# Kernel optimization log

Measured on AMD Instinct MI355X. Metric: run time of the kernel, lower is better.

Reference implementation:

```python
import jax, jax.numpy as jnp
import numpy as np

N, E, D_NODE, D_EDGE, H, NUM_CLASSES = 2048, 4096, 128, 128, 4, 16
SPARSE_RATIO = 0.5  # forward arg sparse_ratio; <1.0 triggers top-k node masking
NEG = jnp.float32(-1e9)


def _mha(x, wq, bq, wk, bk, wv, bv, wo, bo, mask):
    """Multi-head self-attention over tokens x [T, D]; mask broadcastable to [H, T, T]."""
    T, D = x.shape
    dh = D // H
    q = (x @ wq + bq).reshape(T, H, dh)
    k = (x @ wk + bk).reshape(T, H, dh)
    v = (x @ wv + bv).reshape(T, H, dh)
    scores = jnp.einsum('qhd,khd->hqk', q, k) * (1.0 / float(np.sqrt(dh)))
    scores = jnp.where(mask, scores, NEG)
    attn = jax.nn.softmax(scores, axis=-1)
    out = jnp.einsum('hqk,khd->qhd', attn, v).reshape(T, D)
    return out @ wo + bo


def setup_inputs() -> dict:
    key = jax.random.key(0)
    ks = jax.random.split(key, 20)
    f32 = jnp.float32
    def w(i, shape):
        return jax.random.normal(ks[i], shape, dtype=f32) * 0.02
    z = lambda *s: jnp.zeros(s, f32)
    return {
        'node_features': jax.random.normal(ks[0], (N, D_NODE), dtype=f32),
        'edge_features': jax.random.normal(ks[1], (E, D_EDGE), dtype=f32),
        'edge_index': jax.random.randint(ks[2], (2, E), 0, N),
        'w_rn': w(3, (D_NODE, 1)), 'b_rn': z(1),
        'w_re': w(4, (D_EDGE, 1)), 'b_re': z(1),
        'wq_n': w(5, (D_NODE, D_NODE)), 'bq_n': z(D_NODE),
        'wk_n': w(6, (D_NODE, D_NODE)), 'bk_n': z(D_NODE),
        'wv_n': w(7, (D_NODE, D_NODE)), 'bv_n': z(D_NODE),
        'wo_n': w(8, (D_NODE, D_NODE)), 'bo_n': z(D_NODE),
        'wq_e': w(9, (D_EDGE, D_EDGE)), 'bq_e': z(D_EDGE),
        'wk_e': w(10, (D_EDGE, D_EDGE)), 'bk_e': z(D_EDGE),
        'wv_e': w(11, (D_EDGE, D_EDGE)), 'bv_e': z(D_EDGE),
        'wo_e': w(12, (D_EDGE, D_EDGE)), 'bo_e': z(D_EDGE),
        'w_ne': w(13, (D_NODE, D_EDGE)), 'b_ne': z(D_EDGE),
        'w_c1': w(14, (D_EDGE, 2 * D_EDGE)), 'b_c1': z(2 * D_EDGE),
        'w_c2': w(15, (2 * D_EDGE, NUM_CLASSES)), 'b_c2': z(NUM_CLASSES),
    }


def reference(node_features, edge_features, edge_index,
              w_rn, b_rn, w_re, b_re,
              wq_n, bq_n, wk_n, bk_n, wv_n, bv_n, wo_n, bo_n,
              wq_e, bq_e, wk_e, bk_e, wv_e, bv_e, wo_e, bo_e,
              w_ne, b_ne, w_c1, b_c1, w_c2, b_c2):
    # Importance router: scalar sigmoid scores per node / edge
    node_scores = jax.nn.sigmoid(node_features @ w_rn + b_rn)[:, 0]  # [N]
    edge_scores = jax.nn.sigmoid(edge_features @ w_re + b_re)[:, 0]  # [E]
    # Gate features by importance (routing)
    x_n = node_features * node_scores[:, None]
    x_e = edge_features * edge_scores[:, None]
    # Conditional top-k node mask (sparse_ratio < 1.0)
    k = int(SPARSE_RATIO * N)
    thresh = jax.lax.top_k(node_scores, k)[0][-1]
    node_mask = node_scores >= thresh  # [N] bool, keys kept in node attention
    # Edge adjacency (line graph): edges sharing an endpoint attend to each other
    src, dst = edge_index[0], edge_index[1]
    adj = ((src[:, None] == src[None, :]) | (src[:, None] == dst[None, :]) |
           (dst[:, None] == src[None, :]) | (dst[:, None] == dst[None, :]))  # [E, E]
    # Dual parallel attention
    node_out = _mha(x_n, wq_n, bq_n, wk_n, bk_n, wv_n, bv_n, wo_n, bo_n,
                    node_mask[None, None, :])
    edge_out = _mha(x_e, wq_e, bq_e, wk_e, bk_e, wv_e, bv_e, wo_e, bo_e,
                    adj[None, :, :])
    node_msg = node_out[src] + node_out[dst]  # [E, D_NODE] gather at endpoints
    updated_edges = edge_out + node_msg @ w_ne + b_ne  # [E, D_EDGE]
    # Classifier: Linear -> GELU -> Linear
    h = jax.nn.gelu(updated_edges @ w_c1 + b_c1)
    return h @ w_c2 + b_c2  # [E, NUM_CLASSES]
```

## Files before the change

kernel.cpp:

```cpp
#include <hip/hip_runtime.h>
#include <math.h>

#define N_NODES 2048
#define N_EDGES 4096
#define DIM 128
#define HEADS 4
#define DH 32
#define NCLS 16
#define TOPK 1024
#define NBR_CAP 64
#define NSPLIT 4
#define QB 32
#define SCALE 0.17677669529663687f

#define FMA4(ACC, AS, BV)                                       \
  ACC.x = fmaf(AS, BV.x, ACC.x); ACC.y = fmaf(AS, BV.y, ACC.y); \
  ACC.z = fmaf(AS, BV.z, ACC.z); ACC.w = fmaf(AS, BV.w, ACC.w)

__device__ __forceinline__ float wave_reduce_sum(float v) {
#pragma unroll
  for (int o = 32; o > 0; o >>= 1) v += __shfl_xor(v, o, 64);
  return v;
}

__global__ __launch_bounds__(256) void prep_kernel(
    const float* __restrict__ nf, const float* __restrict__ ef,
    const float* __restrict__ w_rn, const float* __restrict__ b_rn,
    const float* __restrict__ w_re, const float* __restrict__ b_re,
    const int* __restrict__ src, const int* __restrict__ dst,
    const float* __restrict__ wo_n, const float* __restrict__ bo_n,
    const float* __restrict__ w_ne, const float* __restrict__ b_ne,
    float* __restrict__ ns, float* __restrict__ es, int* __restrict__ nbr,
    int* __restrict__ deg, float* __restrict__ wfu, float* __restrict__ bfu) {
  int tid = threadIdx.x;
  int bid = blockIdx.x;
  if (bid < 1536) {
    int wid = tid >> 6, lane = tid & 63;
    int row = bid * 4 + wid;
    const float* feat;
    const float* w;
    float b;
    float* scp;
    if (row < N_NODES) {
      feat = nf + (size_t)row * DIM;
      w = w_rn; b = b_rn[0];
      scp = ns + row;
    } else {
      int r = row - N_NODES;
      feat = ef + (size_t)r * DIM;
      w = w_re; b = b_re[0];
      scp = es + r;
    }
    float d = feat[lane] * w[lane] + feat[lane + 64] * w[lane + 64];
    d = wave_reduce_sum(d);
    if (lane == 0) *scp = 1.0f / (1.0f + __expf(-(d + b)));
    return;
  }
  if (bid < 2560) {
    __shared__ int sL[N_EDGES];
    __shared__ int dL[N_EDGES];
    __shared__ int cnt[4];
    int bq = bid - 1536;
#pragma unroll
    for (int i = 0; i < 16; i++) {
      int j = i * 256 + tid;
      sL[j] = src[j];
      dL[j] = dst[j];
    }
    if (tid < 4) cnt[tid] = 0;
    __syncthreads();
    int w = tid >> 6, lane = tid & 63;
    int qi = bq * 4 + w;
    int sq = sL[qi], dq = dL[qi];
    for (int j = lane; j < N_EDGES; j += 64) {
      int sj = sL[j], dj = dL[j];
      if (sj == sq || sj == dq || dj == sq || dj == dq) {
        int pos = atomicAdd(&cnt[w], 1);
        if (pos < NBR_CAP) nbr[(size_t)qi * NBR_CAP + pos] = j;
      }
    }
    __syncthreads();
    if (tid < 4) deg[bq * 4 + tid] = min(cnt[tid], NBR_CAP);
    return;
  }
  if (bid < 2564) {
    __shared__ float As[16][68];
    __shared__ float Bs[16][68];
    int idx = bid - 2560;
    int bm = (idx >> 1) * 64, bn = (idx & 1) * 64;
    int tm = (tid >> 4) * 4, tn = (tid & 15) * 4;
    float4 acc[4] = {{0,0,0,0},{0,0,0,0},{0,0,0,0},{0,0,0,0}};
    for (int k0 = 0; k0 < DIM; k0 += 16) {
#pragma unroll
      for (int i = 0; i < 4; i++) {
        int e = i * 256 + tid;
        int r = e >> 4, kk = e & 15;
        As[kk][r] = wo_n[(size_t)(bm + r) * DIM + k0 + kk];
        int kb = e >> 6, c = e & 63;
        Bs[kb][c] = w_ne[(size_t)(k0 + kb) * DIM + bn + c];
      }
      __syncthreads();
#pragma unroll
      for (int kk = 0; kk < 16; kk++) {
        float4 a = *(const float4*)&As[kk][tm];
        float4 b = *(const float4*)&Bs[kk][tn];
        FMA4(acc[0], a.x, b); FMA4(acc[1], a.y, b);
        FMA4(acc[2], a.z, b); FMA4(acc[3], a.w, b);
      }
      __syncthreads();
    }
#pragma unroll
    for (int i = 0; i < 4; i++)
      *(float4*)&wfu[(size_t)(bm + tm + i) * DIM + bn + tn] = acc[i];
    return;
  }
  if (tid < DIM) {
    float a = 0.f;
    for (int k = 0; k < DIM; k++)
      a = fmaf(bo_n[k], w_ne[(size_t)k * DIM + tid], a);
    bfu[tid] = 2.f * a + b_ne[tid];
  }
}

typedef float As128T[16][136];
typedef float Bs68T[16][68];
__device__ __forceinline__ void gemm_body128(
    As128T& As, Bs68T& Bs, const float* __restrict__ A,
    const float* __restrict__ B, const float* gs, int bm, int bn, int K,
    int N, float4 (&acc)[8], int tid) {
  int g4 = (tid >> 4) * 4, tn = (tid & 15) * 4;
  for (int k0 = 0; k0 < K; k0 += 16) {
#pragma unroll
    for (int i = 0; i < 8; i++) {
      int e = i * 256 + tid;
      int r = e >> 4, kk = e & 15;
      float a = A[(size_t)(bm + r) * K + k0 + kk];
      As[kk][r] = gs ? a * gs[r] : a;
    }
#pragma unroll
    for (int i = 0; i < 4; i++) {
      int e = i * 256 + tid;
      int kb = e >> 6, c = e & 63;
      Bs[kb][c] = B[(size_t)(k0 + kb) * N + bn + c];
    }
    __syncthreads();
#pragma unroll
    for (int kk = 0; kk < 16; kk++) {
      float4 a0 = *(const float4*)&As[kk][g4];
      float4 a1 = *(const float4*)&As[kk][g4 + 64];
      float4 b = *(const float4*)&Bs[kk][tn];
      FMA4(acc[0], a0.x, b); FMA4(acc[1], a0.y, b);
      FMA4(acc[2], a0.z, b); FMA4(acc[3], a0.w, b);
      FMA4(acc[4], a1.x, b); FMA4(acc[5], a1.y, b);
      FMA4(acc[6], a1.z, b); FMA4(acc[7], a1.w, b);
    }
    __syncthreads();
  }
}

__global__ __launch_bounds__(256) void topk_qkv_kernel(
    const float* __restrict__ nf, const float* __restrict__ ef,
    const float* __restrict__ ns, const float* __restrict__ es,
    const float* __restrict__ wq_n, const float* __restrict__ wk_n,
    const float* __restrict__ wv_n, const float* __restrict__ wq_e,
    const float* __restrict__ wk_e, const float* __restrict__ wv_e,
    const float* __restrict__ bq_n, const float* __restrict__ bk_n,
    const float* __restrict__ bv_n, const float* __restrict__ bq_e,
    const float* __restrict__ bk_e, const float* __restrict__ bv_e,
    float* __restrict__ qn, float* __restrict__ kn, float* __restrict__ vn,
    float* __restrict__ qe, float* __restrict__ ke, float* __restrict__ ve,
    int* __restrict__ kidx, int* __restrict__ nkept) {
  __shared__ float As[16][136];
  __shared__ float Bs[16][68];
  __shared__ float ss[128];
  __shared__ unsigned sh_lo;
  __shared__ int wcnt;
  int tid = threadIdx.x;
  if (blockIdx.x == 0) {
    if (tid == 0) wcnt = 0;
    if (tid < 64) {
      unsigned bv[32];
#pragma unroll
      for (int i = 0; i < 32; i++) bv[i] = __float_as_uint(ns[tid * 32 + i]);
      unsigned lo = 0u, hi = 0x3F800000u;
      while (lo < hi) {
        unsigned mid = (unsigned)(((unsigned long long)lo + hi + 1ull) >> 1);
        int c = 0;
#pragma unroll
        for (int i = 0; i < 32; i++) c += (bv[i] >= mid);
#pragma unroll
        for (int o = 1; o < 64; o <<= 1) c += __shfl_xor(c, o, 64);
        if (c >= TOPK) lo = mid; else hi = mid - 1;
      }
      if (tid == 0) sh_lo = lo;
    }
    __syncthreads();
    unsigned lo = sh_lo;
#pragma unroll
    for (int i = 0; i < 8; i++) {
      int idx = tid * 8 + i;
      if (__float_as_uint(ns[idx]) >= lo) kidx[atomicAdd(&wcnt, 1)] = idx;
    }
    __syncthreads();
    if (tid == 0) nkept[0] = wcnt;
    return;
  }
  int bx = blockIdx.x - 1;
  bool edge = bx >= 96;
  int mat, bm, bn;
  const float* A;
  const float* sc;
  if (!edge) {
    mat = bx / 32;
    int rem = bx % 32;
    bm = (rem >> 1) * 128;
    bn = (rem & 1) * 64;
    A = nf; sc = ns;
  } else {
    int be = bx - 96;
    mat = be / 64;
    int rem = be % 64;
    bm = (rem >> 1) * 128;
    bn = (rem & 1) * 64;
    A = ef; sc = es;
  }
  const float* W;
  const float* bias;
  float* C;
  if (!edge) {
    if (mat == 0) { W = wq_n; bias = bq_n; C = qn; }
    else if (mat == 1) { W = wk_n; bias = bk_n; C = kn; }
    else { W = wv_n; bias = bv_n; C = vn; }
  } else {
    if (mat == 0) { W = wq_e; bias = bq_e; C = qe; }
    else if (mat == 1) { W = wk_e; bias = bk_e; C = ke; }
    else { W = wv_e; bias = bv_e; C = ve; }
  }
  if (tid < 128) ss[tid] = sc[bm + tid];
  __syncthreads();
  float4 acc[8] = {{0,0,0,0},{0,0,0,0},{0,0,0,0},{0,0,0,0},
                   {0,0,0,0},{0,0,0,0},{0,0,0,0},{0,0,0,0}};
  gemm_body128(As, Bs, A, W, ss, bm, bn, DIM, DIM, acc, tid);
  int g4 = (tid >> 4) * 4, tn = (tid & 15) * 4;
  float4 b4 = *(const float4*)&bias[bn + tn];
#pragma unroll
  for (int i = 0; i < 4; i++) {
    float4 r;
    r.x = acc[i].x + b4.x; r.y = acc[i].y + b4.y;
    r.z = acc[i].z + b4.z; r.w = acc[i].w + b4.w;
    *(float4*)&C[(size_t)(bm + g4 + i) * DIM + bn + tn] = r;
  }
#pragma unroll
  for (int i = 0; i < 4; i++) {
    float4 r;
    r.x = acc[4 + i].x + b4.x; r.y = acc[4 + i].y + b4.y;
    r.z = acc[4 + i].z + b4.z; r.w = acc[4 + i].w + b4.w;
    *(float4*)&C[(size_t)(bm + 64 + g4 + i) * DIM + bn + tn] = r;
  }
}

__global__ __launch_bounds__(256) void attn_kernel(
    const float* __restrict__ Q, const float* __restrict__ K,
    const float* __restrict__ V, const int* __restrict__ kidx,
    const int* __restrict__ nkeptp, float* __restrict__ pacc,
    float* __restrict__ ps,
    const float* __restrict__ Qe, const float* __restrict__ Ke,
    const float* __restrict__ Ve, const int* __restrict__ nbr,
    const int* __restrict__ deg, float* __restrict__ Oe) {
  __shared__ float Qs[32][36];
  __shared__ float Ks[64][36];
  __shared__ float Vs[64][36];
  __shared__ float Ps[32][68];
  int tid = threadIdx.x;
  int bid = blockIdx.x;
  if (bid < 1024) {
    int bxa = bid & 63;
    int h = (bid >> 6) & 3;
    int sp = bid >> 8;
    int qbase = bxa * QB;
    int nkept = nkeptp[0];
    int spl = (nkept + NSPLIT - 1) / NSPLIT;
    int start = sp * spl;
    int end = min(start + spl, nkept);

    {
      int q8 = tid >> 3, d8 = tid & 7;
      const float4* qp =
          (const float4*)(Q + (size_t)(qbase + q8) * DIM + h * DH) + d8;
      float4 qv = *qp;
      Qs[d8 * 4 + 0][q8] = qv.x;
      Qs[d8 * 4 + 1][q8] = qv.y;
      Qs[d8 * 4 + 2][q8] = qv.z;
      Qs[d8 * 4 + 3][q8] = qv.w;
    }

    int tq = tid >> 5;
    int tk = tid & 31;
    int kg = tid >> 6;
    int tq2 = (tid >> 3) & 7;
    int td4 = tid & 7;
    float4 o4[4] = {{0,0,0,0},{0,0,0,0},{0,0,0,0},{0,0,0,0}};
    float sump[4] = {0.f, 0.f, 0.f, 0.f};

    for (int t0 = start; t0 < end; t0 += 64) {
#pragma unroll
      for (int i = 0; i < 2; i++) {
        int id = i * 256 + tid;
        int r = id >> 3, c4 = id & 7;
        int row = t0 + r;
        int ki = (row < end) ? kidx[row] : kidx[0];
        const float4* kp = (const float4*)(K + (size_t)ki * DIM + h * DH) + c4;
        const float4* vp = (const float4*)(V + (size_t)ki * DIM + h * DH) + c4;
        *(float4*)&Ks[r][c4 * 4] = *kp;
        *(float4*)&Vs[r][c4 * 4] = *vp;
      }
      __syncthreads();
      float4 s0v = {0.f, 0.f, 0.f, 0.f};
      float4 s1v = {0.f, 0.f, 0.f, 0.f};
#pragma unroll
      for (int kk4 = 0; kk4 < 8; kk4++) {
        int kk = kk4 * 4;
        float4 ka = *(const float4*)&Ks[tk][kk];
        float4 kb = *(const float4*)&Ks[tk + 32][kk];
        float4 qa = *(const float4*)&Qs[kk + 0][tq * 4];
        float4 qb = *(const float4*)&Qs[kk + 1][tq * 4];
        float4 qc = *(const float4*)&Qs[kk + 2][tq * 4];
        float4 qd = *(const float4*)&Qs[kk + 3][tq * 4];
        FMA4(s0v, ka.x, qa); FMA4(s0v, ka.y, qb);
        FMA4(s0v, ka.z, qc); FMA4(s0v, ka.w, qd);
        FMA4(s1v, kb.x, qa); FMA4(s1v, kb.y, qb);
        FMA4(s1v, kb.z, qc); FMA4(s1v, kb.w, qd);
      }
      bool va = (t0 + tk) < end;
      bool vb = (t0 + tk + 32) < end;
      float p00 = va ? __expf(s0v.x * SCALE) : 0.f;
      float p01 = va ? __expf(s0v.y * SCALE) : 0.f;
      float p02 = va ? __expf(s0v.z * SCALE) : 0.f;
      float p03 = va ? __expf(s0v.w * SCALE) : 0.f;
      float p10 = vb ? __expf(s1v.x * SCALE) : 0.f;
      float p11 = vb ? __expf(s1v.y * SCALE) : 0.f;
      float p12 = vb ? __expf(s1v.z * SCALE) : 0.f;
      float p13 = vb ? __expf(s1v.w * SCALE) : 0.f;
      Ps[tq * 4 + 0][tk] = p00;      Ps[tq * 4 + 1][tk] = p01;
      Ps[tq * 4 + 2][tk] = p02;      Ps[tq * 4 + 3][tk] = p03;
      Ps[tq * 4 + 0][tk + 32] = p10; Ps[tq * 4 + 1][tk + 32] = p11;
      Ps[tq * 4 + 2][tk + 32] = p12; Ps[tq * 4 + 3][tk + 32] = p13;
      sump[0] += p00 + p10;
      sump[1] += p01 + p11;
      sump[2] += p02 + p12;
      sump[3] += p03 + p13;
      __syncthreads();
#pragma unroll
      for (int k4 = 0; k4 < 4; k4++) {
        int kb = kg * 16 + k4 * 4;
        float4 p0 = *(const float4*)&Ps[tq2 * 4 + 0][kb];
        float4 p1 = *(const float4*)&Ps[tq2 * 4 + 1][kb];
        float4 p2 = *(const float4*)&Ps[tq2 * 4 + 2][kb];
        float4 p3 = *(const float4*)&Ps[tq2 * 4 + 3][kb];
        float4 v0 = *(const float4*)&Vs[kb + 0][td4 * 4];
        float4 v1 = *(const float4*)&Vs[kb + 1][td4 * 4];
        float4 v2 = *(const float4*)&Vs[kb + 2][td4 * 4];
        float4 v3 = *(const float4*)&Vs[kb + 3][td4 * 4];
        FMA4(o4[0], p0.x, v0); FMA4(o4[0], p0.y, v1);
        FMA4(o4[0], p0.z, v2); FMA4(o4[0], p0.w, v3);
        FMA4(o4[1], p1.x, v0); FMA4(o4[1], p1.y, v1);
        FMA4(o4[1], p1.z, v2); FMA4(o4[1], p1.w, v3);
        FMA4(o4[2], p2.x, v0); FMA4(o4[2], p2.y, v1);
        FMA4(o4[2], p2.z, v2); FMA4(o4[2], p2.w, v3);
        FMA4(o4[3], p3.x, v0); FMA4(o4[3], p3.y, v1);
        FMA4(o4[3], p3.z, v2); FMA4(o4[3], p3.w, v3);
      }
      __syncthreads();
    }
#pragma unroll
    for (int os = 1; os < 32; os <<= 1) {
#pragma unroll
      for (int j = 0; j < 4; j++) sump[j] += __shfl_xor(sump[j], os, 64);
    }
    if (tk == 0) {
#pragma unroll
      for (int j = 0; j < 4; j++) {
        int q = qbase + tq * 4 + j;
        size_t idx = ((size_t)q * HEADS + h) * NSPLIT + sp;
        ps[idx] = sump[j];
      }
    }
    float* scrA = &Ks[0][0];
    float* scrB = &Vs[0][0];
    int slot = (kg * 64 + tq2 * 8 + td4) * 8;
    *(float4*)&scrA[slot + 0] = o4[0];
    *(float4*)&scrA[slot + 4] = o4[1];
    *(float4*)&scrB[slot + 0] = o4[2];
    *(float4*)&scrB[slot + 4] = o4[3];
    __syncthreads();
    {
      int qq = tid >> 3;
      int d4 = tid & 7;
      int tqr = qq >> 2, j = qq & 3;
      const float* bank = (j < 2) ? scrA : scrB;
      int off = (j & 1) * 4;
      float4 of = {0.f, 0.f, 0.f, 0.f};
#pragma unroll
      for (int g = 0; g < 4; g++) {
        float4 part =
            *(const float4*)&bank[(g * 64 + tqr * 8 + d4) * 8 + off];
        of.x += part.x; of.y += part.y; of.z += part.z; of.w += part.w;
      }
      size_t idx = ((size_t)(qbase + qq) * HEADS + h) * NSPLIT + sp;
      *(float4*)&pacc[idx * 32 + d4 * 4] = of;
    }
    return;
  }
  int h = tid >> 6;
  int lane = tid & 63;
  int ql = lane >> 4, j4 = (lane >> 2) & 3, g = lane & 3;
  int qi = (bid - 1024) * 4 + ql;
  int dg = deg[qi];
  const float4* qp = (const float4*)(Qe + (size_t)qi * DIM + h * DH + g * 8);
  float4 q0 = qp[0], q1 = qp[1];
  float s = 0.f;
  float4 a0 = make_float4(0.f, 0.f, 0.f, 0.f);
  float4 a1 = make_float4(0.f, 0.f, 0.f, 0.f);
  for (int c0 = 0; c0 < dg; c0 += 4) {
    int j = c0 + j4;
    bool act = j < dg;
    int ei = act ? nbr[(size_t)qi * NBR_CAP + j] : 0;
    const float4* kp = (const float4*)(Ke + (size_t)ei * DIM + h * DH + g * 8);
    float4 k0 = kp[0], k1 = kp[1];
    float pd = q0.x * k0.x + q0.y * k0.y + q0.z * k0.z + q0.w * k0.w +
               q1.x * k1.x + q1.y * k1.y + q1.z * k1.z + q1.w * k1.w;
    pd += __shfl_xor(pd, 1, 64);
    pd += __shfl_xor(pd, 2, 64);
    float pr = act ? __expf(pd * SCALE) : 0.f;
    s += pr;
    const float4* vp = (const float4*)(Ve + (size_t)ei * DIM + h * DH + g * 8);
    float4 v0 = vp[0], v1 = vp[1];
    FMA4(a0, pr, v0);
    FMA4(a1, pr, v1);
  }
#pragma unroll
  for (int o = 4; o <= 8; o <<= 1) {
    s += __shfl_xor(s, o, 64);
    a0.x += __shfl_xor(a0.x, o, 64); a0.y += __shfl_xor(a0.y, o, 64);
    a0.z += __shfl_xor(a0.z, o, 64); a0.w += __shfl_xor(a0.w, o, 64);
    a1.x += __shfl_xor(a1.x, o, 64); a1.y += __shfl_xor(a1.y, o, 64);
    a1.z += __shfl_xor(a1.z, o, 64); a1.w += __shfl_xor(a1.w, o, 64);
  }
  if (j4 == 0) {
    float inv = 1.0f / s;
    float4* op = (float4*)(Oe + (size_t)qi * DIM + h * DH + g * 8);
    float4 r0 = {a0.x * inv, a0.y * inv, a0.z * inv, a0.w * inv};
    float4 r1 = {a1.x * inv, a1.y * inv, a1.z * inv, a1.w * inv};
    op[0] = r0;
    op[1] = r1;
  }
}

__global__ __launch_bounds__(256) void attn_reduce_kernel(
    const float* __restrict__ pacc, const float* __restrict__ ps,
    float* __restrict__ O) {
  int gid = blockIdx.x * 256 + threadIdx.x;
  int qh = gid >> 5, d = gid & 31;
  int q = qh >> 2, h = qh & 3;
  float ssum = 0.f, v = 0.f;
#pragma unroll
  for (int sp = 0; sp < NSPLIT; sp++) {
    size_t idx = (size_t)qh * NSPLIT + sp;
    ssum += ps[idx];
    v += pacc[idx * 32 + d];
  }
  O[(size_t)q * DIM + h * DH + d] = v / ssum;
}

__global__ __launch_bounds__(256) void tail_kernel(
    const float* __restrict__ aoe, const float* __restrict__ wo_e,
    const float* __restrict__ bo_e, const float* __restrict__ aon,
    const int* __restrict__ src, const int* __restrict__ dst,
    const float* __restrict__ wfu, const float* __restrict__ bfu,
    const float* __restrict__ w_c1, const float* __restrict__ b_c1,
    float* __restrict__ hb) {
  __shared__ __align__(16) char smem[21120];
  float (*ue_s)[132] = (float(*)[132])smem;
  float (*As0)[12] = (float(*)[12])(smem + 4224);
  float (*Bs)[132] = (float(*)[132])(smem + 4992);
  float (*Bs2)[264] = (float(*)[264])(smem + 4224);
  int tid = threadIdx.x;
  int bm = blockIdx.x * 8;
  int tr = tid >> 5;
  int tn = (tid & 31) * 4;
  float4 acc = {0, 0, 0, 0};
  for (int k0 = 0; k0 < DIM; k0 += 16) {
    if (tid < 128) {
      int r = tid >> 4, kk = tid & 15;
      As0[kk][r] = aoe[(size_t)(bm + r) * DIM + k0 + kk];
    }
#pragma unroll
    for (int i = 0; i < 8; i++) {
      int id = i * 256 + tid;
      int kb = id >> 7, c = id & 127;
      Bs[kb][c] = wo_e[(size_t)(k0 + kb) * DIM + c];
    }
    __syncthreads();
#pragma unroll
    for (int kk = 0; kk < 16; kk++) {
      float a = As0[kk][tr];
      float4 b = *(const float4*)&Bs[kk][tn];
      FMA4(acc, a, b);
    }
    __syncthreads();
  }
  for (int k0 = 0; k0 < DIM; k0 += 16) {
    if (tid < 128) {
      int r = tid >> 4, kk = tid & 15;
      int row = bm + r;
      int s0 = src[row], d0 = dst[row];
      As0[kk][r] = aon[(size_t)s0 * DIM + k0 + kk] +
                   aon[(size_t)d0 * DIM + k0 + kk];
    }
#pragma unroll
    for (int i = 0; i < 8; i++) {
      int id = i * 256 + tid;
      int kb = id >> 7, c = id & 127;
      Bs[kb][c] = wfu[(size_t)(k0 + kb) * DIM + c];
    }
    __syncthreads();
#pragma unroll
    for (int kk = 0; kk < 16; kk++) {
      float a = As0[kk][tr];
      float4 b = *(const float4*)&Bs[kk][tn];
      FMA4(acc, a, b);
    }
    __syncthreads();
  }
  {
    float4 be = *(const float4*)&bo_e[tn];
    float4 bf = *(const float4*)&bfu[tn];
    float4 r;
    r.x = acc.x + be.x + bf.x; r.y = acc.y + be.y + bf.y;
    r.z = acc.z + be.z + bf.z; r.w = acc.w + be.w + bf.w;
    *(float4*)&ue_s[tr][tn] = r;
  }
  __syncthreads();
  int c4 = (tid & 31) * 4;
  float4 acc2[2] = {{0,0,0,0},{0,0,0,0}};
  for (int k0 = 0; k0 < DIM; k0 += 16) {
#pragma unroll
    for (int i = 0; i < 16; i++) {
      int id = i * 256 + tid;
      int kb = id >> 8, c = id & 255;
      Bs2[kb][c] = w_c1[(size_t)(k0 + kb) * 256 + c];
    }
    __syncthreads();
#pragma unroll
    for (int kk = 0; kk < 16; kk++) {
      float av = ue_s[tr][k0 + kk];
      float4 bva = *(const float4*)&Bs2[kk][c4];
      float4 bvb = *(const float4*)&Bs2[kk][c4 + 128];
      FMA4(acc2[0], av, bva);
      FMA4(acc2[1], av, bvb);
    }
    __syncthreads();
  }
  float4 bc0 = *(const float4*)&b_c1[c4];
  float4 bc1 = *(const float4*)&b_c1[c4 + 128];
#pragma unroll
  for (int half = 0; half < 2; half++) {
    float4 bb = half ? bc1 : bc0;
    float4 av = acc2[half];
    float vv[4] = {av.x + bb.x, av.y + bb.y, av.z + bb.z, av.w + bb.w};
#pragma unroll
    for (int j = 0; j < 4; j++) {
      float v = vv[j];
      float u = 0.7978845608028654f * (v + 0.044715f * v * v * v);
      vv[j] = 0.5f * v * (1.0f + tanhf(u));
    }
    float4 r = {vv[0], vv[1], vv[2], vv[3]};
    *(float4*)&hb[(size_t)(bm + tr) * 256 + c4 + half * 128] = r;
  }
}

__global__ __launch_bounds__(256) void gemm_out_kernel(
    const float* __restrict__ Hm, const float* __restrict__ B,
    const float* __restrict__ bias, float* __restrict__ C) {
  __shared__ float Bs[256 * 16];
  __shared__ float red[256];
  int tid = threadIdx.x;
#pragma unroll
  for (int i = 0; i < 16; i++) Bs[i * 256 + tid] = B[i * 256 + tid];
  __syncthreads();
  int row = blockIdx.x * 8 + ((tid >> 4) & 7);
  int col = tid & 15;
  int half = tid >> 7;
  const float* hp = Hm + (size_t)row * 256 + half * 128;
  float sacc = half ? 0.f : bias[col];
#pragma unroll 8
  for (int k = 0; k < 128; k++)
    sacc = fmaf(hp[k], Bs[(half * 128 + k) * 16 + col], sacc);
  red[tid] = sacc;
  __syncthreads();
  if (tid < 128)
    C[(size_t)row * NCLS + col] = red[tid] + red[tid + 128];
}

extern "C" void kernel_launch(void* const* d_in, const int* in_sizes, int n_in,
                              void* d_out, int out_size, void* d_ws,
                              size_t ws_size, hipStream_t stream) {
  const float* nf = (const float*)d_in[0];
  const float* ef = (const float*)d_in[1];
  const int* ei = (const int*)d_in[2];
  const float* w_rn = (const float*)d_in[3];
  const float* b_rn = (const float*)d_in[4];
  const float* w_re = (const float*)d_in[5];
  const float* b_re = (const float*)d_in[6];
  const float* wq_n = (const float*)d_in[7];
  const float* bq_n = (const float*)d_in[8];
  const float* wk_n = (const float*)d_in[9];
  const float* bk_n = (const float*)d_in[10];
  const float* wv_n = (const float*)d_in[11];
  const float* bv_n = (const float*)d_in[12];
  const float* wo_n = (const float*)d_in[13];
  const float* bo_n = (const float*)d_in[14];
  const float* wq_e = (const float*)d_in[15];
  const float* bq_e = (const float*)d_in[16];
  const float* wk_e = (const float*)d_in[17];
  const float* bk_e = (const float*)d_in[18];
  const float* wv_e = (const float*)d_in[19];
  const float* bv_e = (const float*)d_in[20];
  const float* wo_e = (const float*)d_in[21];
  const float* bo_e = (const float*)d_in[22];
  const float* w_ne = (const float*)d_in[23];
  const float* b_ne = (const float*)d_in[24];
  const float* w_c1 = (const float*)d_in[25];
  const float* b_c1 = (const float*)d_in[26];
  const float* w_c2 = (const float*)d_in[27];
  const float* b_c2 = (const float*)d_in[28];

  const int* src = ei;
  const int* dst = ei + N_EDGES;

  float* ws = (float*)d_ws;
  size_t o = 0;
  float* ns = ws + o;   o += 2048;
  float* es = ws + o;   o += 4096;
  int* kidx = (int*)(ws + o); o += 2048;
  int* nkept = (int*)(ws + o); o += 64;
  int* nbr = (int*)(ws + o); o += (size_t)N_EDGES * NBR_CAP;
  int* degp = (int*)(ws + o); o += N_EDGES;
  float* wfu = ws + o;  o += DIM * DIM;
  float* bfu = ws + o;  o += DIM;
  float* qn = ws + o;   o += (size_t)N_NODES * DIM;
  float* kn = ws + o;   o += (size_t)N_NODES * DIM;
  float* vn = ws + o;   o += (size_t)N_NODES * DIM;
  float* qe = ws + o;   o += (size_t)N_EDGES * DIM;
  float* ke = ws + o;   o += (size_t)N_EDGES * DIM;
  float* ve = ws + o;   o += (size_t)N_EDGES * DIM;
  float* aon = ws + o;  o += (size_t)N_NODES * DIM;
  float* aoe = ws + o;  o += (size_t)N_EDGES * DIM;
  float* hb = ws + o;   o += (size_t)N_EDGES * 2 * DIM;
  float* ps = ws + o;   o += (size_t)N_NODES * HEADS * NSPLIT;
  float* pacc = hb;

  prep_kernel<<<dim3(2565), 256, 0, stream>>>(
      nf, ef, w_rn, b_rn, w_re, b_re, src, dst, wo_n, bo_n, w_ne, b_ne,
      ns, es, nbr, degp, wfu, bfu);
  topk_qkv_kernel<<<dim3(289), 256, 0, stream>>>(
      nf, ef, ns, es, wq_n, wk_n, wv_n, wq_e, wk_e, wv_e,
      bq_n, bk_n, bv_n, bq_e, bk_e, bv_e, qn, kn, vn, qe, ke, ve,
      kidx, nkept);
  attn_kernel<<<dim3(2048), 256, 0, stream>>>(
      qn, kn, vn, kidx, nkept, pacc, ps, qe, ke, ve, nbr, degp, aoe);
  attn_reduce_kernel<<<dim3(N_NODES * HEADS * DH / 256), 256, 0, stream>>>(
      pacc, ps, aon);
  tail_kernel<<<dim3(N_EDGES / 8), 256, 0, stream>>>(
      aoe, wo_e, bo_e, aon, src, dst, wfu, bfu, w_c1, b_c1, hb);
  gemm_out_kernel<<<dim3(N_EDGES / 8), 256, 0, stream>>>(hb, w_c2, b_c2,
                                                         (float*)d_out);
}
```

Before: 108.1 us.

## Fuse split-attention reduce into attn kernel and classifier output into tail

The separate attention split-reduce kernel is removed. The last-arriving split block of each (query block, head) group, detected with an atomic counter and threadfence, now does the normalisation and writes the node attention output. The final 256->16 classifier GEMM is folded into the tail kernel: the GELU activations stay in registers, w_c2 is transposed into shared memory, and results are reduced with wave shuffles, so the hidden buffer is never written to or read back from global memory. This drops two kernel launches and a global round trip, in exchange for atomics, fences and extra shuffle work in the tail.

```diff
diff --git a/kernel.cpp b/kernel.cpp
--- a/kernel.cpp
+++ b/kernel.cpp
@@ -31,7 +31,8 @@
     const float* __restrict__ wo_n, const float* __restrict__ bo_n,
     const float* __restrict__ w_ne, const float* __restrict__ b_ne,
     float* __restrict__ ns, float* __restrict__ es, int* __restrict__ nbr,
-    int* __restrict__ deg, float* __restrict__ wfu, float* __restrict__ bfu) {
+    int* __restrict__ deg, float* __restrict__ wfu, float* __restrict__ bfu,
+    int* __restrict__ acnt) {
   int tid = threadIdx.x;
   int bid = blockIdx.x;
   if (bid < 1536) {
@@ -114,6 +115,7 @@
       *(float4*)&wfu[(size_t)(bm + tm + i) * DIM + bn + tn] = acc[i];
     return;
   }
+  acnt[tid] = 0;
   if (tid < DIM) {
     float a = 0.f;
     for (int k = 0; k < DIM; k++)
@@ -263,7 +265,7 @@
     const float* __restrict__ Q, const float* __restrict__ K,
     const float* __restrict__ V, const int* __restrict__ kidx,
     const int* __restrict__ nkeptp, float* __restrict__ pacc,
-    float* __restrict__ ps,
+    float* __restrict__ ps, int* __restrict__ acnt, float* __restrict__ aon,
     const float* __restrict__ Qe, const float* __restrict__ Ke,
     const float* __restrict__ Ve, const int* __restrict__ nbr,
     const int* __restrict__ deg, float* __restrict__ Oe) {
@@ -271,12 +273,14 @@
   __shared__ float Ks[64][36];
   __shared__ float Vs[64][36];
   __shared__ float Ps[32][68];
+  __shared__ int isLast;
   int tid = threadIdx.x;
   int bid = blockIdx.x;
   if (bid < 1024) {
     int bxa = bid & 63;
     int h = (bid >> 6) & 3;
     int sp = bid >> 8;
+    int grp = bid & 255;
     int qbase = bxa * QB;
     int nkept = nkeptp[0];
     int spl = (nkept + NSPLIT - 1) / NSPLIT;
@@ -409,6 +413,30 @@
       size_t idx = ((size_t)(qbase + qq) * HEADS + h) * NSPLIT + sp;
       *(float4*)&pacc[idx * 32 + d4 * 4] = of;
     }
+    __syncthreads();
+    if (tid == 0) {
+      __threadfence();
+      int old = atomicAdd(&acnt[grp], 1);
+      isLast = (old == NSPLIT - 1);
+    }
+    __syncthreads();
+    if (!isLast) return;
+    __threadfence();
+#pragma unroll
+    for (int i = 0; i < 4; i++) {
+      int e = i * 256 + tid;
+      int qq = e >> 5, d = e & 31;
+      int q = qbase + qq;
+      float ssum = 0.f, v = 0.f;
+#pragma unroll
+      for (int s2 = 0; s2 < NSPLIT; s2++) {
+        size_t idx = ((size_t)q * HEADS + h) * NSPLIT + s2;
+        ssum += ps[idx];
+        v += pacc[idx * 32 + d];
+      }
+      aon[(size_t)q * DIM + h * DH + d] = v / ssum;
+    }
+    if (tid == 0) acnt[grp] = 0;
     return;
   }
   int h = tid >> 6;
@@ -456,34 +484,20 @@
   }
 }
 
-__global__ __launch_bounds__(256) void attn_reduce_kernel(
-    const float* __restrict__ pacc, const float* __restrict__ ps,
-    float* __restrict__ O) {
-  int gid = blockIdx.x * 256 + threadIdx.x;
-  int qh = gid >> 5, d = gid & 31;
-  int q = qh >> 2, h = qh & 3;
-  float ssum = 0.f, v = 0.f;
-#pragma unroll
-  for (int sp = 0; sp < NSPLIT; sp++) {
-    size_t idx = (size_t)qh * NSPLIT + sp;
-    ssum += ps[idx];
-    v += pacc[idx * 32 + d];
-  }
-  O[(size_t)q * DIM + h * DH + d] = v / ssum;
-}
-
 __global__ __launch_bounds__(256) void tail_kernel(
     const float* __restrict__ aoe, const float* __restrict__ wo_e,
     const float* __restrict__ bo_e, const float* __restrict__ aon,
     const int* __restrict__ src, const int* __restrict__ dst,
     const float* __restrict__ wfu, const float* __restrict__ bfu,
     const float* __restrict__ w_c1, const float* __restrict__ b_c1,
-    float* __restrict__ hb) {
+    const float* __restrict__ w_c2, const float* __restrict__ b_c2,
+    float* __restrict__ out) {
   __shared__ __align__(16) char smem[21120];
   float (*ue_s)[132] = (float(*)[132])smem;
   float (*As0)[12] = (float(*)[12])(smem + 4224);
   float (*Bs)[132] = (float(*)[132])(smem + 4992);
   float (*Bs2)[264] = (float(*)[264])(smem + 4224);
+  float* wT = (float*)(smem + 4224);
   int tid = threadIdx.x;
   int bm = blockIdx.x * 8;
   int tr = tid >> 5;
@@ -561,45 +575,59 @@
     }
     __syncthreads();
   }
-  float4 bc0 = *(const float4*)&b_c1[c4];
-  float4 bc1 = *(const float4*)&b_c1[c4 + 128];
-#pragma unroll
-  for (int half = 0; half < 2; half++) {
-    float4 bb = half ? bc1 : bc0;
-    float4 av = acc2[half];
-    float vv[4] = {av.x + bb.x, av.y + bb.y, av.z + bb.z, av.w + bb.w};
-#pragma unroll
-    for (int j = 0; j < 4; j++) {
-      float v = vv[j];
-      float u = 0.7978845608028654f * (v + 0.044715f * v * v * v);
-      vv[j] = 0.5f * v * (1.0f + tanhf(u));
-    }
-    float4 r = {vv[0], vv[1], vv[2], vv[3]};
-    *(float4*)&hb[(size_t)(bm + tr) * 256 + c4 + half * 128] = r;
-  }
-}
-
-__global__ __launch_bounds__(256) void gemm_out_kernel(
-    const float* __restrict__ Hm, const float* __restrict__ B,
-    const float* __restrict__ bias, float* __restrict__ C) {
-  __shared__ float Bs[256 * 16];
-  __shared__ float red[256];
-  int tid = threadIdx.x;
-#pragma unroll
-  for (int i = 0; i < 16; i++) Bs[i * 256 + tid] = B[i * 256 + tid];
+  float hv[2][4];
+  {
+    float4 bc0 = *(const float4*)&b_c1[c4];
+    float4 bc1 = *(const float4*)&b_c1[c4 + 128];
+#pragma unroll
+    for (int half = 0; half < 2; half++) {
+      float4 bb = half ? bc1 : bc0;
+      float4 av = acc2[half];
+      float vv[4] = {av.x + bb.x, av.y + bb.y, av.z + bb.z, av.w + bb.w};
+#pragma unroll
+      for (int j = 0; j < 4; j++) {
+        float v = vv[j];
+        float u = 0.7978845608028654f * (v + 0.044715f * v * v * v);
+        hv[half][j] = 0.5f * v * (1.0f + tanhf(u));
+      }
+    }
+  }
   __syncthreads();
-  int row = blockIdx.x * 8 + ((tid >> 4) & 7);
-  int col = tid & 15;
-  int half = tid >> 7;
-  const float* hp = Hm + (size_t)row * 256 + half * 128;
-  float sacc = half ? 0.f : bias[col];
-#pragma unroll 8
-  for (int k = 0; k < 128; k++)
-    sacc = fmaf(hp[k], Bs[(half * 128 + k) * 16 + col], sacc);
-  red[tid] = sacc;
+#pragma unroll
+  for (int i = 0; i < 4; i++) {
+    int id = i * 256 + tid;
+    float4 w4 = ((const float4*)w_c2)[id];
+    int k = id >> 2, cc = (id & 3) * 4;
+    wT[(cc + 0) * 260 + k] = w4.x;
+    wT[(cc + 1) * 260 + k] = w4.y;
+    wT[(cc + 2) * 260 + k] = w4.z;
+    wT[(cc + 3) * 260 + k] = w4.w;
+  }
   __syncthreads();
-  if (tid < 128)
-    C[(size_t)row * NCLS + col] = red[tid] + red[tid + 128];
+  float oacc[NCLS];
+#pragma unroll
+  for (int c = 0; c < NCLS; c++) {
+    float4 wa = *(const float4*)&wT[c * 260 + c4];
+    float4 wb = *(const float4*)&wT[c * 260 + c4 + 128];
+    float v = hv[0][0] * wa.x;
+    v = fmaf(hv[0][1], wa.y, v);
+    v = fmaf(hv[0][2], wa.z, v);
+    v = fmaf(hv[0][3], wa.w, v);
+    v = fmaf(hv[1][0], wb.x, v);
+    v = fmaf(hv[1][1], wb.y, v);
+    v = fmaf(hv[1][2], wb.z, v);
+    v = fmaf(hv[1][3], wb.w, v);
+    oacc[c] = v;
+  }
+#pragma unroll
+  for (int os = 1; os < 32; os <<= 1) {
+#pragma unroll
+    for (int c = 0; c < NCLS; c++) oacc[c] += __shfl_xor(oacc[c], os, 64);
+  }
+  if ((tid & 31) < NCLS) {
+    int col = tid & 15;
+    out[(size_t)(bm + tr) * NCLS + col] = oacc[col] + b_c2[col];
+  }
 }
 
 extern "C" void kernel_launch(void* const* d_in, const int* in_sizes, int n_in,
@@ -656,23 +684,21 @@
   float* ve = ws + o;   o += (size_t)N_EDGES * DIM;
   float* aon = ws + o;  o += (size_t)N_NODES * DIM;
   float* aoe = ws + o;  o += (size_t)N_EDGES * DIM;
-  float* hb = ws + o;   o += (size_t)N_EDGES * 2 * DIM;
+  float* pacc = ws + o; o += (size_t)N_NODES * HEADS * NSPLIT * DH;
   float* ps = ws + o;   o += (size_t)N_NODES * HEADS * NSPLIT;
-  float* pacc = hb;
+  int* acnt = (int*)(ws + o); o += 256;
 
   prep_kernel<<<dim3(2565), 256, 0, stream>>>(
       nf, ef, w_rn, b_rn, w_re, b_re, src, dst, wo_n, bo_n, w_ne, b_ne,
-      ns, es, nbr, degp, wfu, bfu);
+      ns, es, nbr, degp, wfu, bfu, acnt);
   topk_qkv_kernel<<<dim3(289), 256, 0, stream>>>(
       nf, ef, ns, es, wq_n, wk_n, wv_n, wq_e, wk_e, wv_e,
       bq_n, bk_n, bv_n, bq_e, bk_e, bv_e, qn, kn, vn, qe, ke, ve,
       kidx, nkept);
   attn_kernel<<<dim3(2048), 256, 0, stream>>>(
-      qn, kn, vn, kidx, nkept, pacc, ps, qe, ke, ve, nbr, degp, aoe);
-  attn_reduce_kernel<<<dim3(N_NODES * HEADS * DH / 256), 256, 0, stream>>>(
-      pacc, ps, aon);
+      qn, kn, vn, kidx, nkept, pacc, ps, acnt, aon, qe, ke, ve, nbr, degp,
+      aoe);
   tail_kernel<<<dim3(N_EDGES / 8), 256, 0, stream>>>(
-      aoe, wo_e, bo_e, aon, src, dst, wfu, bfu, w_c1, b_c1, hb);
-  gemm_out_kernel<<<dim3(N_EDGES / 8), 256, 0, stream>>>(hb, w_c2, b_c2,
-                                                         (float*)d_out);
+      aoe, wo_e, bo_e, aon, src, dst, wfu, bfu, w_c1, b_c1, w_c2, b_c2,
+      (float*)d_out);
 }
```

After: 186.8 us. +72.9%, slower.
